# Performance work log

Measured on AMD Instinct MI355X. Metric: run time of the kernel, lower is better.

Reference implementation:

```python
import jax, jax.numpy as jnp
import numpy as np

WS = 7      # window_size
SS = 3      # shift_size
NH = 12     # num_heads
HD = 32     # head_dim (dim // num_heads)


def _ln(x, g, b, eps=1e-5):
    mu = jnp.mean(x, axis=-1, keepdims=True)
    var = jnp.mean((x - mu) ** 2, axis=-1, keepdims=True)
    return (x - mu) * jax.lax.rsqrt(var + eps) * g + b


def setup_inputs() -> dict:
    key = jax.random.key(0)
    ks = jax.random.split(key, 8)
    b, h, w, c = 32, 56, 56, 384
    hid = 4 * c
    s = 0.02
    return {
        "x": jax.random.normal(ks[0], (b, h * w, c), jnp.float32),
        "h": h,
        "w": w,
        "g1": jnp.ones((c,), jnp.float32),
        "b1": jnp.zeros((c,), jnp.float32),
        "wqkv": jax.random.normal(ks[1], (c, 3 * c), jnp.float32) * s,
        "bqkv": jnp.zeros((3 * c,), jnp.float32),
        "wproj": jax.random.normal(ks[2], (c, c), jnp.float32) * s,
        "bproj": jnp.zeros((c,), jnp.float32),
        "g2": jnp.ones((c,), jnp.float32),
        "b2": jnp.zeros((c,), jnp.float32),
        "wfc1": jax.random.normal(ks[3], (c, hid), jnp.float32) * s,
        "bfc1": jnp.zeros((hid,), jnp.float32),
        "wfc2": jax.random.normal(ks[4], (hid, c), jnp.float32) * s,
        "bfc2": jnp.zeros((c,), jnp.float32),
    }


def _swin_block(x, h, w, g1, b1, wqkv, bqkv, wproj, bproj, g2, b2, wfc1, bfc1, wfc2, bfc2):
    b, l, c = x.shape
    shortcut = x
    xn = _ln(x, g1, b1).reshape(b, h, w, c)
    pad_h = (WS - h % WS) % WS
    pad_w = (WS - w % WS) % WS
    if pad_h > 0 or pad_w > 0:
        xn = jnp.pad(xn, ((0, 0), (0, pad_h), (0, pad_w), (0, 0)))
    hp, wp = xn.shape[1], xn.shape[2]
    if SS > 0:
        xn = jnp.roll(xn, (-SS, -SS), axis=(1, 2))
    # window partition -> [b*nw, ws*ws, c]
    win = xn.reshape(b, hp // WS, WS, wp // WS, WS, c)
    win = win.transpose(0, 1, 3, 2, 4, 5).reshape(-1, WS * WS, c)
    # window attention
    bnw, n, _ = win.shape
    qkv = (win @ wqkv + bqkv).reshape(bnw, n, 3, NH, HD)
    q, k, v = qkv[:, :, 0], qkv[:, :, 1], qkv[:, :, 2]  # [bnw, n, nh, hd]
    scale = HD ** -0.5
    attn = jnp.einsum("bqhd,bkhd->bhqk", q, k) * scale
    attn = jax.nn.softmax(attn, axis=-1)
    out = jnp.einsum("bhqk,bkhd->bqhd", attn, v).reshape(bnw, n, c)
    out = out @ wproj + bproj
    # window reverse
    xo = out.reshape(b, hp // WS, wp // WS, WS, WS, c)
    xo = xo.transpose(0, 1, 3, 2, 4, 5).reshape(b, hp, wp, c)
    if SS > 0:
        xo = jnp.roll(xo, (SS, SS), axis=(1, 2))
    if pad_h > 0 or pad_w > 0:
        xo = xo[:, :h, :w, :]
    xo = xo.reshape(b, h * w, c)
    xo = shortcut + xo
    # MLP with residual
    y = _ln(xo, g2, b2)
    y = jax.nn.gelu(y @ wfc1 + bfc1, approximate=False) @ wfc2 + bfc2
    return xo + y


def reference(x, h, w, g1, b1, wqkv, bqkv, wproj, bproj, g2, b2, wfc1, bfc1, wfc2, bfc2):
    return _swin_block(x, h, w, g1, b1, wqkv, bqkv, wproj, bproj,
                       g2, b2, wfc1, bfc1, wfc2, bfc2)
```

## Files before the change

### kernel.cpp

```cpp
#include <hip/hip_runtime.h>
#include <math.h>


typedef float f32x4 __attribute__((ext_vector_type(4)));
typedef float f32x2 __attribute__((ext_vector_type(2)));
typedef __bf16 bf16x8 __attribute__((ext_vector_type(8)));
typedef short s16x8 __attribute__((ext_vector_type(8)));
typedef unsigned short u16x2 __attribute__((ext_vector_type(2)));

#define DEV static __device__ __forceinline__

DEV unsigned short f2bf(float f) {
  unsigned int u = __builtin_bit_cast(unsigned int, f);
  u += 0x7fffu + ((u >> 16) & 1u);
  return (unsigned short)(u >> 16);
}
DEV float bf2f(unsigned short h) {
  unsigned int u = ((unsigned int)h) << 16;
  return __builtin_bit_cast(float, u);
}
DEV void load_lds16(const void* g, void* l) {
  __builtin_amdgcn_global_load_lds(
      (const __attribute__((address_space(1))) unsigned int*)g,
      (__attribute__((address_space(3))) unsigned int*)l, 16, 0, 0);
}

DEV int win_src_row(int row) {
  int win = row / 49, t = row - win * 49;
  int bimg = win >> 6, wrem = win & 63;
  int wy = wrem >> 3, wx = wrem & 7;
  int ti = t / 7, tj = t - ti * 7;
  int hh = wy * 7 + ti, ww = wx * 7 + tj;
  int sh = hh + 3; if (sh >= 56) sh -= 56;
  int sw = ww + 3; if (sw >= 56) sw -= 56;
  return bimg * 3136 + sh * 56 + sw;
}

__global__ void wt_kernel(const float* __restrict__ w, unsigned short* __restrict__ wt,
                          int Kd, int Nd) {
  int idx = blockIdx.x * 256 + threadIdx.x;
  if (idx >= Kd * Nd) return;
  int n = idx / Kd, k = idx - n * Kd;
  wt[idx] = f2bf(w[(size_t)k * Nd + n]);
}

template <int GATHER>
__global__ __launch_bounds__(256) void ln_kernel(const float* __restrict__ x,
                                                 const float* __restrict__ g,
                                                 const float* __restrict__ bb,
                                                 unsigned short* __restrict__ out) {
  int row = blockIdx.x * 4 + (threadIdx.x >> 6);
  int lane = threadIdx.x & 63;
  int src = GATHER ? win_src_row(row) : row;
  const float* xr = x + (size_t)src * 384;
  f32x2 p0 = *(const f32x2*)(xr + lane * 2);
  f32x2 p1 = *(const f32x2*)(xr + 128 + lane * 2);
  f32x2 p2 = *(const f32x2*)(xr + 256 + lane * 2);
  float s = p0.x + p0.y + p1.x + p1.y + p2.x + p2.y;
  float s2 = p0.x * p0.x + p0.y * p0.y + p1.x * p1.x + p1.y * p1.y +
             p2.x * p2.x + p2.y * p2.y;
#pragma unroll
  for (int off = 32; off; off >>= 1) {
    s += __shfl_xor(s, off);
    s2 += __shfl_xor(s2, off);
  }
  float mu = s * (1.0f / 384.0f);
  float rs = rsqrtf(s2 * (1.0f / 384.0f) - mu * mu + 1e-5f);
  unsigned short* orow = out + (size_t)row * 384;
  int c = lane * 2;
  u16x2 o;
  o.x = f2bf((p0.x - mu) * rs * g[c] + bb[c]);
  o.y = f2bf((p0.y - mu) * rs * g[c + 1] + bb[c + 1]);
  *(u16x2*)(orow + c) = o;
  c += 128;
  o.x = f2bf((p1.x - mu) * rs * g[c] + bb[c]);
  o.y = f2bf((p1.y - mu) * rs * g[c + 1] + bb[c + 1]);
  *(u16x2*)(orow + c) = o;
  c += 128;
  o.x = f2bf((p2.x - mu) * rs * g[c] + bb[c]);
  o.y = f2bf((p2.y - mu) * rs * g[c + 1] + bb[c + 1]);
  *(u16x2*)(orow + c) = o;
}

template <int EPI>
__global__ __launch_bounds__(512, 4) void gemmP(const unsigned short* __restrict__ A,
                                                const unsigned short* __restrict__ BT,
                                                const float* __restrict__ bias, int Kd,
                                                int nTilesN, void* __restrict__ out0,
                                                const float* __restrict__ res) {
  constexpr int BM = 256, BN = 128, BK = 32;
  __shared__ __attribute__((aligned(16))) unsigned short As[3][BM * BK];
  __shared__ __attribute__((aligned(16))) unsigned short Bs[3][BN * BK];
  const int tid = threadIdx.x;
  const int wid = tid >> 6, lane = tid & 63;
  const int nwg = gridDim.x;
  const int xcd = blockIdx.x & 7, loc = blockIdx.x >> 3;
  const int q = nwg >> 3, rr = nwg & 7;
  const int swz = (xcd < rr ? xcd * (q + 1) : rr * (q + 1) + (xcd - rr) * q) + loc;
  const int bm = swz / nTilesN, bn = swz - bm * nTilesN;
  const int wr = wid >> 1, wc = wid & 1;
  f32x4 acc[4][4] = {};
  const int srow = tid >> 2;
  const int chunk = (tid & 3) ^ ((tid >> 3) & 3);
  const unsigned short* gA0 = A + (size_t)(bm * BM + srow) * Kd + chunk * 8;
  const unsigned short* gB0 = BT + (size_t)(bn * BN + srow) * Kd + chunk * 8;
  const size_t rowstep = (size_t)128 * Kd;

  auto STAGE = [&](int b, int t) {
    const int k0 = t << 5;
    unsigned short* lA = &As[b][tid * 8];
    load_lds16(gA0 + k0, lA);
    load_lds16(gA0 + k0 + rowstep, lA + 4096);
    load_lds16(gB0 + k0, &Bs[b][tid * 8]);
  };

  const int frow = lane & 15, g = lane >> 4;
  const int rslot = (g ^ ((frow >> 1) & 3)) << 3;
  const int aBase = (wr * 64 + frow) * BK + rslot;
  const int bBase = (wc * 64 + frow) * BK + rslot;

  const int nk = Kd >> 5;
  STAGE(0, 0);
  STAGE(1, 1);
  int b = 0;
  for (int t = 0; t < nk; ++t) {
    __builtin_amdgcn_sched_barrier(0);
    if (t + 1 < nk) asm volatile("s_waitcnt vmcnt(3)");
    else asm volatile("s_waitcnt vmcnt(0)");
    __builtin_amdgcn_sched_barrier(0);
    __builtin_amdgcn_s_barrier();
    __builtin_amdgcn_sched_barrier(0);
    if (t + 2 < nk) STAGE(b == 0 ? 2 : b - 1, t + 2);
    __builtin_amdgcn_sched_barrier(0);
    const unsigned short* Ab = As[b];
    const unsigned short* Bb = Bs[b];
    bf16x8 bfr[4], af[4];
#pragma unroll
    for (int n = 0; n < 4; n++) bfr[n] = *(const bf16x8*)(Bb + bBase + n * 16 * BK);
#pragma unroll
    for (int m = 0; m < 4; m++) af[m] = *(const bf16x8*)(Ab + aBase + m * 16 * BK);
    __builtin_amdgcn_s_setprio(1);
#pragma unroll
    for (int m = 0; m < 4; m++)
#pragma unroll
      for (int n = 0; n < 4; n++)
        acc[m][n] = __builtin_amdgcn_mfma_f32_16x16x32_bf16(af[m], bfr[n],
                                                            acc[m][n], 0, 0, 0);
    __builtin_amdgcn_s_setprio(0);
    b = (b == 2) ? 0 : b + 1;
  }
  const int rbase = bm * BM + wr * 64 + (g << 2);
  const int cbase = bn * BN + wc * 64 + frow;
#pragma unroll
  for (int m = 0; m < 4; m++) {
#pragma unroll
    for (int j = 0; j < 4; j++) {
      const int r = rbase + m * 16 + j;
      if constexpr (EPI == 0) {
        unsigned short* C = (unsigned short*)out0;
        size_t ro = (size_t)r * 1152;
#pragma unroll
        for (int n = 0; n < 4; n++) {
          int cc = cbase + n * 16;
          C[ro + cc] = f2bf(acc[m][n][j] + bias[cc]);
        }
      } else if constexpr (EPI == 1) {
        float* XO = (float*)out0;
        size_t srowo = (size_t)win_src_row(r) * 384;
#pragma unroll
        for (int n = 0; n < 4; n++) {
          int cc = cbase + n * 16;
          XO[srowo + cc] = acc[m][n][j] + bias[cc] + res[srowo + cc];
        }
      } else if constexpr (EPI == 2) {
        unsigned short* H1 = (unsigned short*)out0;
        size_t ro = (size_t)r * 1536;
#pragma unroll
        for (int n = 0; n < 4; n++) {
          int cc = cbase + n * 16;
          float u = acc[m][n][j] + bias[cc];
          H1[ro + cc] = f2bf(0.5f * u * (1.0f + erff(u * 0.70710678118654752f)));
        }
      } else {
        float* O = (float*)out0;
        size_t ro = (size_t)r * 384;
#pragma unroll
        for (int n = 0; n < 4; n++) {
          int cc = cbase + n * 16;
          O[ro + cc] = acc[m][n][j] + bias[cc] + res[ro + cc];
        }
      }
    }
  }
}

__global__ __launch_bounds__(256) void attn_mfma(const unsigned short* __restrict__ QKV,
                                                 unsigned short* __restrict__ AO) {
  __shared__ __attribute__((aligned(16))) unsigned short L[4][7168];
  const int wid = threadIdx.x >> 6, lane = threadIdx.x & 63;
  const int blk = blockIdx.x * 4 + wid;
  const int win = blk / 12, head = blk - win * 12;
  unsigned short* Qs = L[wid];
  unsigned short* Ks = Qs + 2048;
  unsigned short* VT = Qs + 4096;
  unsigned short* Ps = Qs + 6144;
  const unsigned short* Qp = QKV + (size_t)win * 49 * 1152 + head * 32;
  for (int i = lane; i < 196; i += 64) {
    int row = i >> 2, c8 = (i & 3) << 3;
    const unsigned short* base = Qp + (size_t)row * 1152 + c8;
    *(s16x8*)(Qs + row * 32 + c8) = *(const s16x8*)(base);
    *(s16x8*)(Ks + row * 32 + c8) = *(const s16x8*)(base + 384);
    s16x8 vv = *(const s16x8*)(base + 768);
#pragma unroll
    for (int u = 0; u < 8; u++) VT[(c8 + u) * 64 + row] = (unsigned short)vv[u];
  }
  if (lane < 60) {
    s16x8 z = {};
    *(s16x8*)(Qs + 1568 + lane * 8) = z;
    *(s16x8*)(Ks + 1568 + lane * 8) = z;
  }
  for (int i = lane; i < 480; i += 64) {
    int d = i / 15, k = 49 + (i - d * 15);
    VT[d * 64 + k] = 0;
  }
  __syncthreads();

  const int g = lane >> 4, qi = lane & 15;
  const float scale = 0.17677669529663689f;
  bf16x8 kf[4];
#pragma unroll
  for (int mt = 0; mt < 4; mt++)
    kf[mt] = *(const bf16x8*)(Ks + (mt * 16 + qi) * 32 + g * 8);

  for (int nt = 0; nt < 4; nt++) {
    bf16x8 qf = *(const bf16x8*)(Qs + (nt * 16 + qi) * 32 + g * 8);
    f32x4 st[4];
#pragma unroll
    for (int mt = 0; mt < 4; mt++) {
      f32x4 zz = {};
      st[mt] = __builtin_amdgcn_mfma_f32_16x16x32_bf16(kf[mt], qf, zz, 0, 0, 0);
    }
    float m = -1e30f;
#pragma unroll
    for (int mt = 0; mt < 3; mt++)
#pragma unroll
      for (int j = 0; j < 4; j++) m = fmaxf(m, st[mt][j]);
    if (g == 0) m = fmaxf(m, st[3][0]);
    m = fmaxf(m, __shfl_xor(m, 16));
    m = fmaxf(m, __shfl_xor(m, 32));
    m *= scale;
    float p[4][4];
    float sum = 0.f;
#pragma unroll
    for (int mt = 0; mt < 4; mt++)
#pragma unroll
      for (int j = 0; j < 4; j++) {
        int k = mt * 16 + g * 4 + j;
        float e = (k < 49) ? __expf(st[mt][j] * scale - m) : 0.f;
        p[mt][j] = e;
        sum += e;
      }
    sum += __shfl_xor(sum, 16);
    sum += __shfl_xor(sum, 32);
    float inv = 1.0f / sum;
#pragma unroll
    for (int mt = 0; mt < 4; mt++)
#pragma unroll
      for (int j = 0; j < 4; j += 2) {
        unsigned int pk = (unsigned int)f2bf(p[mt][j]) |
                          ((unsigned int)f2bf(p[mt][j + 1]) << 16);
        *(unsigned int*)(Ps + qi * 64 + mt * 16 + g * 4 + j) = pk;
      }
    __syncthreads();
    f32x4 acc0 = {}, acc1 = {};
#pragma unroll
    for (int kt = 0; kt < 2; kt++) {
      bf16x8 pa = *(const bf16x8*)(Ps + qi * 64 + kt * 32 + g * 8);
      bf16x8 vb0 = *(const bf16x8*)(VT + qi * 64 + kt * 32 + g * 8);
      bf16x8 vb1 = *(const bf16x8*)(VT + (16 + qi) * 64 + kt * 32 + g * 8);
      acc0 = __builtin_amdgcn_mfma_f32_16x16x32_bf16(pa, vb0, acc0, 0, 0, 0);
      acc1 = __builtin_amdgcn_mfma_f32_16x16x32_bf16(pa, vb1, acc1, 0, 0, 0);
    }
#pragma unroll
    for (int jr = 0; jr < 4; jr++) {
      int q2 = g * 4 + jr;
      int qg = nt * 16 + q2;
      float iv = __shfl(inv, q2);
      if (qg < 49) {
        unsigned short* op = AO + ((size_t)win * 49 + qg) * 384 + head * 32 + qi;
        op[0] = f2bf(acc0[jr] * iv);
        op[16] = f2bf(acc1[jr] * iv);
      }
    }
    __syncthreads();
  }
}

extern "C" void kernel_launch(void* const* d_in, const int* in_sizes, int n_in,
                              void* d_out, int out_size, void* d_ws, size_t ws_size,
                              hipStream_t stream) {
  (void)in_sizes; (void)n_in; (void)out_size; (void)ws_size;
  const float* x = (const float*)d_in[0];
  const float* g1 = (const float*)d_in[3];
  const float* b1 = (const float*)d_in[4];
  const float* wqkv = (const float*)d_in[5];
  const float* bqkv = (const float*)d_in[6];
  const float* wproj = (const float*)d_in[7];
  const float* bproj = (const float*)d_in[8];
  const float* g2 = (const float*)d_in[9];
  const float* b2 = (const float*)d_in[10];
  const float* wfc1 = (const float*)d_in[11];
  const float* bfc1 = (const float*)d_in[12];
  const float* wfc2 = (const float*)d_in[13];
  const float* bfc2 = (const float*)d_in[14];

  char* ws = (char*)d_ws;
  unsigned short* wqkvT = (unsigned short*)ws;
  unsigned short* wprojT = wqkvT + 442368;
  unsigned short* wfc1T = wprojT + 147456;
  unsigned short* wfc2T = wfc1T + 589824;
  unsigned short* XW = wfc2T + 589824;
  unsigned short* QKV = XW + 38535168;
  unsigned short* AOb = XW;
  unsigned short* XN2 = QKV;
  unsigned short* H1buf = QKV + 38535168;
  float* XO = (float*)d_out;
  float* out = (float*)d_out;

  wt_kernel<<<1728, 256, 0, stream>>>(wqkv, wqkvT, 384, 1152);
  wt_kernel<<<576, 256, 0, stream>>>(wproj, wprojT, 384, 384);
  wt_kernel<<<2304, 256, 0, stream>>>(wfc1, wfc1T, 384, 1536);
  wt_kernel<<<2304, 256, 0, stream>>>(wfc2, wfc2T, 1536, 384);

  ln_kernel<1><<<25088, 256, 0, stream>>>(x, g1, b1, XW);
  gemmP<0><<<392 * 9, 512, 0, stream>>>(XW, wqkvT, bqkv, 384, 9, QKV, nullptr);
  attn_mfma<<<6144, 256, 0, stream>>>(QKV, AOb);
  gemmP<1><<<392 * 3, 512, 0, stream>>>(AOb, wprojT, bproj, 384, 3, XO, x);
  ln_kernel<0><<<25088, 256, 0, stream>>>(XO, g2, b2, XN2);
  for (int ch = 0; ch < 2; ch++) {
    const unsigned short* a2 = XN2 + (size_t)ch * 50176 * 384;
    float* o2 = out + (size_t)ch * 50176 * 384;
    gemmP<2><<<196 * 12, 512, 0, stream>>>(a2, wfc1T, bfc1, 384, 12, H1buf, nullptr);
    gemmP<3><<<196 * 3, 512, 0, stream>>>(H1buf, wfc2T, bfc2, 1536, 3, o2, o2);
  }
}
```

Before: 958.1 us.

## Split GEMM main loop into two phases interleaving LDS reads, loads and MFMA

Restructures the triple-buffered bf16 GEMM k-loop into two half-phases. Each phase reads part of the B fragments, issues part of the next-stage global-to-LDS loads, then runs half of the MFMAs, with barriers between phases in a ping-pong style schedule. The aim is to overlap LDS fragment reads and global load issue with MFMA work instead of doing all staging up front. The cost is more workgroup barriers per iteration, and the vmcnt accounting must stay correct with the loads now split across phases.

```diff
diff --git a/kernel.cpp b/kernel.cpp
--- a/kernel.cpp
+++ b/kernel.cpp
@@ -106,47 +106,80 @@
   const unsigned short* gB0 = BT + (size_t)(bn * BN + srow) * Kd + chunk * 8;
   const size_t rowstep = (size_t)128 * Kd;
 
-  auto STAGE = [&](int b, int t) {
-    const int k0 = t << 5;
-    unsigned short* lA = &As[b][tid * 8];
-    load_lds16(gA0 + k0, lA);
-    load_lds16(gA0 + k0 + rowstep, lA + 4096);
-    load_lds16(gB0 + k0, &Bs[b][tid * 8]);
-  };
-
   const int frow = lane & 15, g = lane >> 4;
   const int rslot = (g ^ ((frow >> 1) & 3)) << 3;
   const int aBase = (wr * 64 + frow) * BK + rslot;
   const int bBase = (wc * 64 + frow) * BK + rslot;
 
   const int nk = Kd >> 5;
-  STAGE(0, 0);
-  STAGE(1, 1);
+  {
+    unsigned short* lA = &As[0][tid * 8];
+    load_lds16(gA0, lA);
+    load_lds16(gA0 + rowstep, lA + 4096);
+    load_lds16(gB0, &Bs[0][tid * 8]);
+    unsigned short* lA1 = &As[1][tid * 8];
+    load_lds16(gA0 + 32, lA1);
+    load_lds16(gA0 + 32 + rowstep, lA1 + 4096);
+    load_lds16(gB0 + 32, &Bs[1][tid * 8]);
+  }
+  asm volatile("s_waitcnt vmcnt(3)");
+  __builtin_amdgcn_sched_barrier(0);
+  __builtin_amdgcn_s_barrier();
   int b = 0;
   for (int t = 0; t < nk; ++t) {
-    __builtin_amdgcn_sched_barrier(0);
-    if (t + 1 < nk) asm volatile("s_waitcnt vmcnt(3)");
-    else asm volatile("s_waitcnt vmcnt(0)");
-    __builtin_amdgcn_sched_barrier(0);
-    __builtin_amdgcn_s_barrier();
-    __builtin_amdgcn_sched_barrier(0);
-    if (t + 2 < nk) STAGE(b == 0 ? 2 : b - 1, t + 2);
-    __builtin_amdgcn_sched_barrier(0);
+    const int bst = (b == 0) ? 2 : b - 1;
+    const int k0n = (t + 2) << 5;
     const unsigned short* Ab = As[b];
     const unsigned short* Bb = Bs[b];
-    bf16x8 bfr[4], af[4];
-#pragma unroll
-    for (int n = 0; n < 4; n++) bfr[n] = *(const bf16x8*)(Bb + bBase + n * 16 * BK);
+    __builtin_amdgcn_sched_barrier(0);
+    bf16x8 af[4], bfr[2];
 #pragma unroll
     for (int m = 0; m < 4; m++) af[m] = *(const bf16x8*)(Ab + aBase + m * 16 * BK);
+#pragma unroll
+    for (int n = 0; n < 2; n++) bfr[n] = *(const bf16x8*)(Bb + bBase + n * 16 * BK);
+    if (t + 2 < nk) {
+      unsigned short* lA = &As[bst][tid * 8];
+      load_lds16(gA0 + k0n, lA);
+      load_lds16(gA0 + k0n + rowstep, lA + 4096);
+    }
+    __builtin_amdgcn_sched_barrier(0);
+    __builtin_amdgcn_s_barrier();
+    asm volatile("s_waitcnt lgkmcnt(0)");
+    __builtin_amdgcn_sched_barrier(0);
     __builtin_amdgcn_s_setprio(1);
 #pragma unroll
     for (int m = 0; m < 4; m++)
 #pragma unroll
-      for (int n = 0; n < 4; n++)
+      for (int n = 0; n < 2; n++)
         acc[m][n] = __builtin_amdgcn_mfma_f32_16x16x32_bf16(af[m], bfr[n],
                                                             acc[m][n], 0, 0, 0);
     __builtin_amdgcn_s_setprio(0);
+    __builtin_amdgcn_sched_barrier(0);
+    __builtin_amdgcn_s_barrier();
+    bf16x8 bfr2[2];
+#pragma unroll
+    for (int n = 0; n < 2; n++)
+      bfr2[n] = *(const bf16x8*)(Bb + bBase + (n + 2) * 16 * BK);
+    if (t + 2 < nk) load_lds16(gB0 + k0n, &Bs[bst][tid * 8]);
+    __builtin_amdgcn_sched_barrier(0);
+    __builtin_amdgcn_s_barrier();
+    asm volatile("s_waitcnt lgkmcnt(0)");
+    __builtin_amdgcn_sched_barrier(0);
+    __builtin_amdgcn_s_setprio(1);
+#pragma unroll
+    for (int m = 0; m < 4; m++)
+#pragma unroll
+      for (int n = 0; n < 2; n++)
+        acc[m][n + 2] = __builtin_amdgcn_mfma_f32_16x16x32_bf16(af[m], bfr2[n],
+                                                                acc[m][n + 2], 0, 0, 0);
+    __builtin_amdgcn_s_setprio(0);
+    __builtin_amdgcn_sched_barrier(0);
+    if (t + 1 < nk) {
+      if (t + 2 < nk) asm volatile("s_waitcnt vmcnt(3)");
+      else asm volatile("s_waitcnt vmcnt(0)");
+      __builtin_amdgcn_sched_barrier(0);
+    }
+    __builtin_amdgcn_s_barrier();
     b = (b == 2) ? 0 : b + 1;
   }
   const int rbase = bm * BM + wr * 64 + (g << 2);
```

Result: faster. 909.6 us (-5.1%).
